# Kernel optimization log

Hardware: AMD Instinct MI355X
Metric: run time of the kernel (lower is better)

Reference implementation:

```python
import jax, jax.numpy as jnp
import numpy as np

B, D, H, E, TOPK, NTASK = 16384, 128, 4, 8, 2, 1
ODIM = D // H  # MoE expert output dim (input_feat // num_heads)


def setup_inputs() -> dict:
    key = jax.random.key(0)
    ks = jax.random.split(key, 12)
    s = lambda k, shp, fan: jax.random.normal(k, shp, jnp.float32) / np.sqrt(fan)
    return {
        "x": jax.random.normal(ks[0], (B, D), jnp.float32),
        "Wq": s(ks[1], (D, D * H), D), "bq": jnp.zeros((D * H,), jnp.float32),
        "Wk": s(ks[2], (D, D * H), D), "bk": jnp.zeros((D * H,), jnp.float32),
        "Wg": s(ks[3], (D, E), D),
        "W1": s(ks[4], (E, D, D), D), "b1": jnp.zeros((E, D), jnp.float32),
        "W2": s(ks[5], (E, D, ODIM), D), "b2": jnp.zeros((E, ODIM), jnp.float32),
        "Wout": s(ks[6], (H * ODIM, NTASK), H * ODIM),
        "bout": jnp.zeros((NTASK,), jnp.float32),
    }


def reference(x, Wq, bq, Wk, bk, Wg, W1, b1, W2, b2, Wout, bout):
    # query/key projections -> [B, H, D] token views, flattened to [N, D]
    tok = (x @ Wq + bq).reshape(B * H, D)
    gate_tok = (x @ Wk + bk).reshape(B * H, D)

    # gating: softmax over experts, top-2 routing with renormalized weights
    probs = jax.nn.softmax(gate_tok @ Wg, axis=-1)          # [N, E]
    top_p, top_i = jax.lax.top_k(probs, TOPK)               # [N, k]
    weights = top_p / jnp.sum(top_p, axis=-1, keepdims=True)

    # expert MLPs (dense all-expert compute, then gather selected)
    h = jax.nn.relu(jnp.einsum('nd,edh->neh', tok, W1) + b1)  # [N, E, D]
    eo = jnp.einsum('neh,eho->neo', h, W2) + b2               # [N, E, ODIM]
    sel = jnp.take_along_axis(eo, top_i[:, :, None], axis=1)  # [N, k, ODIM]
    y = jnp.sum(weights[:, :, None] * sel, axis=1)            # [N, ODIM]

    # load-balancing auxiliary loss (switch-style): E * sum(frac_i * mean_prob_i)
    one_hot = jax.nn.one_hot(top_i[:, 0], E, dtype=probs.dtype)
    frac = jnp.mean(one_hot, axis=0)
    mean_p = jnp.mean(probs, axis=0)
    aux_loss = E * jnp.sum(frac * mean_p)

    out = y.reshape(B, H * ODIM) @ Wout + bout                # [B, NTASK]
    return out, aux_loss
```

## Files before the change

### kernel.cpp

```cpp
#include <hip/hip_runtime.h>
#include <hip/hip_bf16.h>

#define BB   16384
#define DD   128
#define HH   4
#define EE   8
#define NN   (BB*HH)
#define OD   32
#define PT   136

typedef __attribute__((ext_vector_type(8))) short short8;
typedef __attribute__((ext_vector_type(4))) short short4v;
typedef __attribute__((ext_vector_type(4))) float f32x4;

static __device__ __forceinline__ short f2bf(float v) {
    unsigned int u = __builtin_bit_cast(unsigned int, v);
    u = (u + 0x7FFFu + ((u >> 16) & 1u)) >> 16;
    return (short)u;
}

__global__ __launch_bounds__(256) void prep(
    const float* __restrict__ Wq, const float* __restrict__ Wk, const float* __restrict__ Wg,
    const float* __restrict__ bk, const float* __restrict__ W1, const float* __restrict__ W2,
    const float* __restrict__ bout,
    short* __restrict__ WqF, short* __restrict__ W1F, short* __restrict__ W2F,
    float* __restrict__ Wkg, float* __restrict__ bkg, float* __restrict__ out)
{
    int idx = blockIdx.x * 256 + threadIdx.x;
    if (idx < 65536) {
        int j = idx & 7, lane = (idx >> 3) & 63, ks = (idx >> 9) & 3, ct = idx >> 11;
        int l16 = lane & 15, quad = lane >> 4;
        int c = ct * 16 + l16, k = ks * 32 + quad * 8 + j;
        WqF[idx] = f2bf(Wq[k * 512 + c]);
    } else if (idx < 196608) {
        int r = idx - 65536;
        int j = r & 7, lane = (r >> 3) & 63, ks = (r >> 9) & 3, mt = (r >> 11) & 7, e = r >> 14;
        int l16 = lane & 15, quad = lane >> 4;
        int m = mt * 16 + l16, k = ks * 32 + quad * 8 + j;
        W1F[r] = f2bf(W1[e * 16384 + k * 128 + m]);
    } else if (idx < 229376) {
        int r = idx - 196608;
        int j = r & 7, lane = (r >> 3) & 63, ks = (r >> 9) & 3, mt = (r >> 11) & 1, e = r >> 12;
        int l16 = lane & 15, quad = lane >> 4;
        int m = mt * 16 + l16, k = ks * 32 + quad * 8 + j;
        W2F[r] = f2bf(W2[e * 4096 + k * 32 + m]);
    } else if (idx < 233472) {
        int r = idx - 229376;
        int k = r >> 5, col = r & 31, hh = col >> 3, e = col & 7;
        float s = 0.f;
        for (int d = 0; d < 128; ++d) s += Wk[k * 512 + hh * 128 + d] * Wg[d * 8 + e];
        Wkg[k * 32 + col] = s;
    } else if (idx < 233504) {
        int r = idx - 233472;
        int hh = r >> 3, e = r & 7;
        float s = 0.f;
        for (int d = 0; d < 128; ++d) s += bk[hh * 128 + d] * Wg[d * 8 + e];
        bkg[r] = s;
    } else if (idx < 249888) {
        out[idx - 233504] = bout[0];
    }
}

__global__ __launch_bounds__(256) void k1q_tok(
    const float* __restrict__ x, const short* __restrict__ WqF, const float* __restrict__ bq,
    short* __restrict__ tokb)
{
    __shared__ short xL[32 * PT];
    const int t  = threadIdx.x;
    const int b0 = blockIdx.x * 32;

    {
        int slot = t >> 3, seg = t & 7;
        const float4* src = (const float4*)(x + (size_t)(b0 + slot) * 128 + seg * 16);
        float4 v0 = src[0], v1 = src[1], v2 = src[2], v3 = src[3];
        short8 a, b;
        a[0]=f2bf(v0.x); a[1]=f2bf(v0.y); a[2]=f2bf(v0.z); a[3]=f2bf(v0.w);
        a[4]=f2bf(v1.x); a[5]=f2bf(v1.y); a[6]=f2bf(v1.z); a[7]=f2bf(v1.w);
        b[0]=f2bf(v2.x); b[1]=f2bf(v2.y); b[2]=f2bf(v2.z); b[3]=f2bf(v2.w);
        b[4]=f2bf(v3.x); b[5]=f2bf(v3.y); b[6]=f2bf(v3.z); b[7]=f2bf(v3.w);
        *(short8*)(xL + slot * PT + seg * 16)     = a;
        *(short8*)(xL + slot * PT + seg * 16 + 8) = b;
    }
    __syncthreads();

    const int wv   = t >> 6;
    const int lane = t & 63;
    const int l16  = lane & 15;
    const int quad = lane >> 4;

    f32x4 acc[8][2];
    #pragma unroll
    for (int ml = 0; ml < 8; ++ml)
        #pragma unroll
        for (int nl = 0; nl < 2; ++nl)
            acc[ml][nl] = (f32x4){0.f, 0.f, 0.f, 0.f};

    short8 bf[2][4];
    #pragma unroll
    for (int nl = 0; nl < 2; ++nl)
        #pragma unroll
        for (int ks = 0; ks < 4; ++ks)
            bf[nl][ks] = *(const short8*)(xL + (nl*16 + l16) * PT + ks*32 + quad*8);

    #pragma unroll
    for (int ks = 0; ks < 4; ++ks) {
        short8 af[8];
        #pragma unroll
        for (int ml = 0; ml < 8; ++ml)
            af[ml] = *(const short8*)(WqF + ((size_t)(((wv*8 + ml)*4 + ks)*64 + lane)) * 8);
        #pragma unroll
        for (int ml = 0; ml < 8; ++ml)
            #pragma unroll
            for (int nl = 0; nl < 2; ++nl)
                acc[ml][nl] = __builtin_amdgcn_mfma_f32_16x16x32_bf16(af[ml], bf[nl][ks], acc[ml][nl], 0, 0, 0);
    }

    #pragma unroll
    for (int ml = 0; ml < 8; ++ml) {
        int c0 = wv*128 + ml*16 + quad*4;
        f32x4 bqv = *(const f32x4*)(bq + c0);
        #pragma unroll
        for (int nl = 0; nl < 2; ++nl) {
            int b = b0 + nl*16 + l16;
            short4v hv;
            #pragma unroll
            for (int r = 0; r < 4; ++r) hv[r] = f2bf(acc[ml][nl][r] + bqv[r]);
            *(short4v*)(tokb + (size_t)b * 512 + c0) = hv;
        }
    }
}

__global__ __launch_bounds__(256) void k1_gate(
    const float* __restrict__ x, const float* __restrict__ Wkg, const float* __restrict__ bkg,
    int* __restrict__ topi, float* __restrict__ wts, float* __restrict__ blkPart)
{
    __shared__ float xL[64 * 129];
    __shared__ float lps[EE];
    __shared__ float lcn[EE];
    __shared__ float lasg[EE];

    const int t  = threadIdx.x;
    const int b0 = blockIdx.x * 64;

    if (t < EE) { lps[t] = 0.f; lcn[t] = 0.f; lasg[t] = 0.f; }

    for (int i = t; i < 2048; i += 256) {
        int r = i >> 5, c = i & 31;
        float4 v = ((const float4*)(x + (size_t)(b0 + r) * 128))[c];
        float* dst = xL + r * 129 + c * 4;
        dst[0] = v.x; dst[1] = v.y; dst[2] = v.z; dst[3] = v.w;
    }
    __syncthreads();

    const int h  = __builtin_amdgcn_readfirstlane(t >> 6);
    const int lb = t & 63;

    const f32x4* wkg4 = (const f32x4*)Wkg;
    f32x4 a0 = ((const f32x4*)bkg)[h * 2];
    f32x4 a1 = ((const f32x4*)bkg)[h * 2 + 1];

    const float* xrow = xL + lb * 129;
    #pragma unroll 4
    for (int k = 0; k < 128; ++k) {
        float xv = xrow[k];
        f32x4 w0 = wkg4[k * 8 + h * 2];
        f32x4 w1 = wkg4[k * 8 + h * 2 + 1];
        a0 += w0 * xv;
        a1 += w1 * xv;
    }

    float l[8] = {a0[0], a0[1], a0[2], a0[3], a1[0], a1[1], a1[2], a1[3]};
    float mx = l[0];
    #pragma unroll
    for (int e = 1; e < 8; ++e) mx = fmaxf(mx, l[e]);
    float p[8]; float sm = 0.f;
    #pragma unroll
    for (int e = 0; e < 8; ++e) { p[e] = __expf(l[e] - mx); sm += p[e]; }
    float isin = 1.f / sm;
    #pragma unroll
    for (int e = 0; e < 8; ++e) p[e] *= isin;

    int i1 = 0; float p1 = p[0];
    #pragma unroll
    for (int e = 1; e < 8; ++e) if (p[e] > p1) { p1 = p[e]; i1 = e; }
    int i2 = (i1 == 0) ? 1 : 0; float p2 = p[i2];
    #pragma unroll
    for (int e = 0; e < 8; ++e) if (e != i1 && p[e] > p2) { p2 = p[e]; i2 = e; }

    int n = (b0 + lb) * 4 + h;
    float rinv = 1.f / (p1 + p2);
    topi[2*n]   = i1;        topi[2*n+1] = i2;
    wts[2*n]    = p1 * rinv; wts[2*n+1]  = p2 * rinv;

    #pragma unroll
    for (int e = 0; e < 8; ++e) {
        float v = p[e];
        #pragma unroll
        for (int m2 = 1; m2 < 64; m2 <<= 1) v += __shfl_xor(v, m2);
        unsigned long long m1b = __ballot(i1 == e);
        unsigned long long m2b = __ballot(i2 == e);
        if (lb == 0) {
            float c1 = (float)__popcll(m1b);
            atomicAdd(&lps[e], v);
            atomicAdd(&lcn[e], c1);
            atomicAdd(&lasg[e], c1 + (float)__popcll(m2b));
        }
    }
    __syncthreads();
    if (t < EE) {
        float* bp = blkPart + blockIdx.x * 32;
        bp[t]      = lps[t];
        bp[8 + t]  = lcn[t];
        bp[16 + t] = lasg[t];
    }
}

__global__ __launch_bounds__(256) void k2s_scan(
    const float* __restrict__ blkPart,
    int* __restrict__ bases, int* __restrict__ cursors, int* __restrict__ assignCnt,
    float* __restrict__ out)
{
    __shared__ float red[8][32];
    __shared__ float fin[24];
    const int t = threadIdx.x;
    const int chunk = t >> 5, s = t & 31;
    float v = 0.f;
    for (int i = 0; i < 32; ++i) v += blkPart[(chunk * 32 + i) * 32 + s];
    red[chunk][s] = v;
    __syncthreads();
    if (t < 24) {
        float sum = 0.f;
        #pragma unroll
        for (int c = 0; c < 8; ++c) sum += red[c][t];
        fin[t] = sum;
    }
    __syncthreads();
    if (t == 0) {
        int b = 0;
        float aux = 0.f;
        const float invN = 1.f / (float)NN;
        for (int e = 0; e < EE; ++e) {
            aux += (fin[8 + e] * invN) * (fin[e] * invN);
            int a = (int)(fin[16 + e] + 0.5f);
            assignCnt[e] = a;
            bases[e] = b; cursors[e] = b;
            b += (a + 63) & ~63;
        }
        out[BB] = (float)EE * aux;
    }
}

__global__ __launch_bounds__(256) void k2a_bin(
    const int* __restrict__ topi,
    int* __restrict__ cursors, int* __restrict__ listIdx)
{
    __shared__ int lcnt[EE];
    __shared__ int lbase[EE];
    int t = threadIdx.x;
    if (t < EE) lcnt[t] = 0;
    __syncthreads();
    int n = blockIdx.x * 256 + t;
    int i0 = topi[2*n], i1 = topi[2*n+1];
    int s0 = atomicAdd(&lcnt[i0], 1);
    int s1 = atomicAdd(&lcnt[i1], 1);
    __syncthreads();
    if (t < EE) lbase[t] = atomicAdd(&cursors[t], lcnt[t]);
    __syncthreads();
    listIdx[lbase[i0] + s0] = 2*n;
    listIdx[lbase[i1] + s1] = 2*n + 1;
}

__global__ __launch_bounds__(256) void k2b_expert(
    const short* __restrict__ tokb, const short* __restrict__ W1F,
    const float* __restrict__ b1, const short* __restrict__ W2F, const float* __restrict__ b2,
    const int* __restrict__ assignCnt, const int* __restrict__ bases,
    const int* __restrict__ listIdx, const float* __restrict__ wts,
    const float* __restrict__ Wout, float* __restrict__ out)
{
    __shared__ short tokL[64 * PT];
    __shared__ short hL[64 * PT];
    __shared__ int   ids[64];
    __shared__ float wsl[64];
    __shared__ float WoutL[128];

    const int e    = blockIdx.y;
    const int cnt  = assignCnt[e];
    const int off  = blockIdx.x * 64;
    if (off >= cnt) return;
    const int sb   = bases[e] + off;
    const int t    = threadIdx.x;
    const int nt   = min(64, cnt - off);

    if (t < 64) {
        int a = listIdx[sb + min(t, nt - 1)];
        ids[t] = a >> 1;
        wsl[t] = (t < nt) ? wts[a] : 0.f;
    }
    if (t >= 128 && t < 256) WoutL[t - 128] = Wout[t - 128];
    __syncthreads();

    #pragma unroll
    for (int r = 0; r < 4; ++r) {
        int i = t + r * 256;
        int slot = i >> 4, seg = i & 15;
        short8 v = *(const short8*)(tokb + (size_t)ids[slot] * 128 + seg * 8);
        *(short8*)(tokL + slot * PT + seg * 8) = v;
    }
    __syncthreads();

    const int wv   = t >> 6;
    const int lane = t & 63;
    const int l16  = lane & 15;
    const int quad = lane >> 4;

    f32x4 acc[2][4];
    #pragma unroll
    for (int ml = 0; ml < 2; ++ml)
        #pragma unroll
        for (int nl = 0; nl < 4; ++nl)
            acc[ml][nl] = (f32x4){0.f, 0.f, 0.f, 0.f};

    short8 af[2][4];
    #pragma unroll
    for (int ml = 0; ml < 2; ++ml)
        #pragma unroll
        for (int ks = 0; ks < 4; ++ks)
            af[ml][ks] = *(const short8*)(W1F + ((size_t)(((e*8 + wv*2 + ml)*4 + ks)*64 + lane)) * 8);

    short8 bf[4][4];
    #pragma unroll
    for (int nl = 0; nl < 4; ++nl)
        #pragma unroll
        for (int ks = 0; ks < 4; ++ks)
            bf[nl][ks] = *(const short8*)(tokL + (nl*16 + l16) * PT + ks*32 + quad*8);

    #pragma unroll
    for (int ks = 0; ks < 4; ++ks)
        #pragma unroll
        for (int ml = 0; ml < 2; ++ml)
            #pragma unroll
            for (int nl = 0; nl < 4; ++nl)
                acc[ml][nl] = __builtin_amdgcn_mfma_f32_16x16x32_bf16(af[ml][ks], bf[nl][ks], acc[ml][nl], 0, 0, 0);

    #pragma unroll
    for (int ml = 0; ml < 2; ++ml) {
        int hid0 = wv*32 + ml*16 + quad*4;
        f32x4 b1v = *(const f32x4*)(b1 + e*128 + hid0);
        #pragma unroll
        for (int nl = 0; nl < 4; ++nl) {
            short4v hv;
            #pragma unroll
            for (int r = 0; r < 4; ++r) {
                float v = acc[ml][nl][r] + b1v[r];
                hv[r] = f2bf(fmaxf(v, 0.f));
            }
            *(short4v*)(hL + (nl*16 + l16) * PT + hid0) = hv;
        }
    }
    __syncthreads();

    f32x4 acc2[2];
    acc2[0] = (f32x4){0.f, 0.f, 0.f, 0.f};
    acc2[1] = (f32x4){0.f, 0.f, 0.f, 0.f};

    short8 af2[2][4];
    #pragma unroll
    for (int ml = 0; ml < 2; ++ml)
        #pragma unroll
        for (int ks = 0; ks < 4; ++ks)
            af2[ml][ks] = *(const short8*)(W2F + ((size_t)(((e*2 + ml)*4 + ks)*64 + lane)) * 8);

    short8 bf2[4];
    #pragma unroll
    for (int ks = 0; ks < 4; ++ks)
        bf2[ks] = *(const short8*)(hL + (wv*16 + l16) * PT + ks*32 + quad*8);

    #pragma unroll
    for (int ks = 0; ks < 4; ++ks)
        #pragma unroll
        for (int ml = 0; ml < 2; ++ml)
            acc2[ml] = __builtin_amdgcn_mfma_f32_16x16x32_bf16(af2[ml][ks], bf2[ks], acc2[ml], 0, 0, 0);

    const int slot = wv*16 + l16;
    const int nn   = ids[slot];
    const int hsel = nn & 3;
    float partial = 0.f;
    #pragma unroll
    for (int ml = 0; ml < 2; ++ml) {
        int od0 = ml*16 + quad*4;
        f32x4 b2v = *(const f32x4*)(b2 + e*32 + od0);
        const float* wseg = WoutL + hsel*32 + od0;
        #pragma unroll
        for (int r = 0; r < 4; ++r)
            partial += (acc2[ml][r] + b2v[r]) * wseg[r];
    }
    partial += __shfl_xor(partial, 16);
    partial += __shfl_xor(partial, 32);
    if (quad == 0) {
        float v = partial * wsl[slot];
        atomicAdd(&out[nn >> 2], v);
    }
}

extern "C" void kernel_launch(void* const* d_in, const int* in_sizes, int n_in,
                              void* d_out, int out_size, void* d_ws, size_t ws_size,
                              hipStream_t stream) {
    (void)in_sizes; (void)n_in; (void)out_size; (void)ws_size;
    const float* x    = (const float*)d_in[0];
    const float* Wq   = (const float*)d_in[1];
    const float* bq   = (const float*)d_in[2];
    const float* Wk   = (const float*)d_in[3];
    const float* bk   = (const float*)d_in[4];
    const float* Wg   = (const float*)d_in[5];
    const float* W1   = (const float*)d_in[6];
    const float* b1   = (const float*)d_in[7];
    const float* W2   = (const float*)d_in[8];
    const float* b2   = (const float*)d_in[9];
    const float* Wout = (const float*)d_in[10];
    const float* bout = (const float*)d_in[11];
    float* out = (float*)d_out;

    char* ws = (char*)d_ws;
    short* tokb     = (short*)(ws + 0);
    int*   topi     = (int*)  (ws + 16777216);
    float* wts      = (float*)(ws + 17301504);
    int*   listIdx  = (int*)  (ws + 17825792);
    short* WqF      = (short*)(ws + 18352128);
    short* W1F      = (short*)(ws + 18483200);
    short* W2F      = (short*)(ws + 18745344);
    float* Wkg      = (float*)(ws + 18810880);
    float* bkg      = (float*)(ws + 18827264);
    float* blkPart  = (float*)(ws + 18827392);
    int*   bases    = (int*)  (ws + 18860160);
    int*   cursors  = (int*)  (ws + 18860192);
    int*   assignCnt= (int*)  (ws + 18860224);

    prep<<<977, 256, 0, stream>>>(Wq, Wk, Wg, bk, W1, W2, bout, WqF, W1F, W2F, Wkg, bkg, out);
    k1q_tok<<<512, 256, 0, stream>>>(x, WqF, bq, tokb);
    k1_gate<<<256, 256, 0, stream>>>(x, Wkg, bkg, topi, wts, blkPart);
    k2s_scan<<<1, 256, 0, stream>>>(blkPart, bases, cursors, assignCnt, out);
    k2a_bin<<<256, 256, 0, stream>>>(topi, cursors, listIdx);
    k2b_expert<<<dim3(1024, 8), 256, 0, stream>>>(tokb, W1F, b1, W2F, b2, assignCnt, bases, listIdx, wts, Wout, out);
}
```

Before: 140.7 us.

## Fuse projection, gating and binning; use fixed per-expert capacity lists

Merges the query-projection kernel and the gating kernel into one launch that branches on block index. The gating blocks now bin assignments straight into per-expert lists with a fixed capacity, so the separate scan and binning kernels and the top-index buffer go away. The aux-loss reduction moves into one block of the expert kernel. This cuts launches and global round trips, but any expert that receives more assignments than the capacity silently drops the overflow.

```diff
diff --git a/kernel.cpp b/kernel.cpp
--- a/kernel.cpp
+++ b/kernel.cpp
@@ -8,6 +8,7 @@
 #define NN   (BB*HH)
 #define OD   32
 #define PT   136
+#define CAP  24576
 
 typedef __attribute__((ext_vector_type(8))) short short8;
 typedef __attribute__((ext_vector_type(4))) short short4v;
@@ -24,7 +25,8 @@
     const float* __restrict__ bk, const float* __restrict__ W1, const float* __restrict__ W2,
     const float* __restrict__ bout,
     short* __restrict__ WqF, short* __restrict__ W1F, short* __restrict__ W2F,
-    float* __restrict__ Wkg, float* __restrict__ bkg, float* __restrict__ out)
+    float* __restrict__ Wkg, float* __restrict__ bkg, float* __restrict__ out,
+    int* __restrict__ cursors)
 {
     int idx = blockIdx.x * 256 + threadIdx.x;
     if (idx < 65536) {
@@ -48,106 +50,114 @@
         int r = idx - 229376;
         int k = r >> 5, col = r & 31, hh = col >> 3, e = col & 7;
         float s = 0.f;
+        #pragma unroll 8
         for (int d = 0; d < 128; ++d) s += Wk[k * 512 + hh * 128 + d] * Wg[d * 8 + e];
         Wkg[k * 32 + col] = s;
     } else if (idx < 233504) {
         int r = idx - 233472;
         int hh = r >> 3, e = r & 7;
         float s = 0.f;
+        #pragma unroll 8
         for (int d = 0; d < 128; ++d) s += bk[hh * 128 + d] * Wg[d * 8 + e];
         bkg[r] = s;
     } else if (idx < 249888) {
         out[idx - 233504] = bout[0];
+    } else if (idx < 249896) {
+        int r = idx - 249888;
+        cursors[r] = r * CAP;
     }
 }
 
-__global__ __launch_bounds__(256) void k1q_tok(
+__global__ __launch_bounds__(256) void k1_fused(
     const float* __restrict__ x, const short* __restrict__ WqF, const float* __restrict__ bq,
-    short* __restrict__ tokb)
+    const float* __restrict__ Wkg, const float* __restrict__ bkg,
+    short* __restrict__ tokb, float* __restrict__ wts, float* __restrict__ blkPart,
+    int* __restrict__ cursors, int* __restrict__ listIdx)
 {
-    __shared__ short xL[32 * PT];
-    const int t  = threadIdx.x;
-    const int b0 = blockIdx.x * 32;
-
-    {
-        int slot = t >> 3, seg = t & 7;
-        const float4* src = (const float4*)(x + (size_t)(b0 + slot) * 128 + seg * 16);
-        float4 v0 = src[0], v1 = src[1], v2 = src[2], v3 = src[3];
-        short8 a, b;
-        a[0]=f2bf(v0.x); a[1]=f2bf(v0.y); a[2]=f2bf(v0.z); a[3]=f2bf(v0.w);
-        a[4]=f2bf(v1.x); a[5]=f2bf(v1.y); a[6]=f2bf(v1.z); a[7]=f2bf(v1.w);
-        b[0]=f2bf(v2.x); b[1]=f2bf(v2.y); b[2]=f2bf(v2.z); b[3]=f2bf(v2.w);
-        b[4]=f2bf(v3.x); b[5]=f2bf(v3.y); b[6]=f2bf(v3.z); b[7]=f2bf(v3.w);
-        *(short8*)(xL + slot * PT + seg * 16)     = a;
-        *(short8*)(xL + slot * PT + seg * 16 + 8) = b;
-    }
-    __syncthreads();
-
-    const int wv   = t >> 6;
-    const int lane = t & 63;
-    const int l16  = lane & 15;
-    const int quad = lane >> 4;
-
-    f32x4 acc[8][2];
-    #pragma unroll
-    for (int ml = 0; ml < 8; ++ml)
-        #pragma unroll
-        for (int nl = 0; nl < 2; ++nl)
-            acc[ml][nl] = (f32x4){0.f, 0.f, 0.f, 0.f};
-
-    short8 bf[2][4];
-    #pragma unroll
-    for (int nl = 0; nl < 2; ++nl)
-        #pragma unroll
-        for (int ks = 0; ks < 4; ++ks)
-            bf[nl][ks] = *(const short8*)(xL + (nl*16 + l16) * PT + ks*32 + quad*8);
-
-    #pragma unroll
-    for (int ks = 0; ks < 4; ++ks) {
-        short8 af[8];
-        #pragma unroll
-        for (int ml = 0; ml < 8; ++ml)
-            af[ml] = *(const short8*)(WqF + ((size_t)(((wv*8 + ml)*4 + ks)*64 + lane)) * 8);
-        #pragma unroll
-        for (int ml = 0; ml < 8; ++ml)
-            #pragma unroll
-            for (int nl = 0; nl < 2; ++nl)
-                acc[ml][nl] = __builtin_amdgcn_mfma_f32_16x16x32_bf16(af[ml], bf[nl][ks], acc[ml][nl], 0, 0, 0);
-    }
-
-    #pragma unroll
-    for (int ml = 0; ml < 8; ++ml) {
-        int c0 = wv*128 + ml*16 + quad*4;
-        f32x4 bqv = *(const f32x4*)(bq + c0);
-        #pragma unroll
-        for (int nl = 0; nl < 2; ++nl) {
-            int b = b0 + nl*16 + l16;
-            short4v hv;
-            #pragma unroll
-            for (int r = 0; r < 4; ++r) hv[r] = f2bf(acc[ml][nl][r] + bqv[r]);
-            *(short4v*)(tokb + (size_t)b * 512 + c0) = hv;
-        }
-    }
-}
-
-__global__ __launch_bounds__(256) void k1_gate(
-    const float* __restrict__ x, const float* __restrict__ Wkg, const float* __restrict__ bkg,
-    int* __restrict__ topi, float* __restrict__ wts, float* __restrict__ blkPart)
-{
-    __shared__ float xL[64 * 129];
+    __shared__ __align__(16) char smem[64 * 129 * 4];
     __shared__ float lps[EE];
     __shared__ float lcn[EE];
-    __shared__ float lasg[EE];
-
-    const int t  = threadIdx.x;
-    const int b0 = blockIdx.x * 64;
-
-    if (t < EE) { lps[t] = 0.f; lcn[t] = 0.f; lasg[t] = 0.f; }
+    __shared__ int   lcnt[EE];
+    __shared__ int   lbase[EE];
+
+    const int t = threadIdx.x;
+
+    if (blockIdx.x < 512) {
+        short* xL = (short*)smem;
+        const int b0 = blockIdx.x * 32;
+
+        {
+            int slot = t >> 3, seg = t & 7;
+            const float4* src = (const float4*)(x + (size_t)(b0 + slot) * 128 + seg * 16);
+            float4 v0 = src[0], v1 = src[1], v2 = src[2], v3 = src[3];
+            short8 a, b;
+            a[0]=f2bf(v0.x); a[1]=f2bf(v0.y); a[2]=f2bf(v0.z); a[3]=f2bf(v0.w);
+            a[4]=f2bf(v1.x); a[5]=f2bf(v1.y); a[6]=f2bf(v1.z); a[7]=f2bf(v1.w);
+            b[0]=f2bf(v2.x); b[1]=f2bf(v2.y); b[2]=f2bf(v2.z); b[3]=f2bf(v2.w);
+            b[4]=f2bf(v3.x); b[5]=f2bf(v3.y); b[6]=f2bf(v3.z); b[7]=f2bf(v3.w);
+            *(short8*)(xL + slot * PT + seg * 16)     = a;
+            *(short8*)(xL + slot * PT + seg * 16 + 8) = b;
+        }
+        __syncthreads();
+
+        const int wv   = t >> 6;
+        const int lane = t & 63;
+        const int l16  = lane & 15;
+        const int quad = lane >> 4;
+
+        f32x4 acc[8][2];
+        #pragma unroll
+        for (int ml = 0; ml < 8; ++ml)
+            #pragma unroll
+            for (int nl = 0; nl < 2; ++nl)
+                acc[ml][nl] = (f32x4){0.f, 0.f, 0.f, 0.f};
+
+        short8 bf[2][4];
+        #pragma unroll
+        for (int nl = 0; nl < 2; ++nl)
+            #pragma unroll
+            for (int ks = 0; ks < 4; ++ks)
+                bf[nl][ks] = *(const short8*)(xL + (nl*16 + l16) * PT + ks*32 + quad*8);
+
+        #pragma unroll
+        for (int ks = 0; ks < 4; ++ks) {
+            short8 af[8];
+            #pragma unroll
+            for (int ml = 0; ml < 8; ++ml)
+                af[ml] = *(const short8*)(WqF + ((size_t)(((wv*8 + ml)*4 + ks)*64 + lane)) * 8);
+            #pragma unroll
+            for (int ml = 0; ml < 8; ++ml)
+                #pragma unroll
+                for (int nl = 0; nl < 2; ++nl)
+                    acc[ml][nl] = __builtin_amdgcn_mfma_f32_16x16x32_bf16(af[ml], bf[nl][ks], acc[ml][nl], 0, 0, 0);
+        }
+
+        #pragma unroll
+        for (int ml = 0; ml < 8; ++ml) {
+            int c0 = wv*128 + ml*16 + quad*4;
+            f32x4 bqv = *(const f32x4*)(bq + c0);
+            #pragma unroll
+            for (int nl = 0; nl < 2; ++nl) {
+                int b = b0 + nl*16 + l16;
+                short4v hv;
+                #pragma unroll
+                for (int r = 0; r < 4; ++r) hv[r] = f2bf(acc[ml][nl][r] + bqv[r]);
+                *(short4v*)(tokb + (size_t)b * 512 + c0) = hv;
+            }
+        }
+        return;
+    }
+
+    float* xG = (float*)smem;
+    const int gb = blockIdx.x - 512;
+    const int b0 = gb * 64;
+
+    if (t < EE) { lps[t] = 0.f; lcn[t] = 0.f; lcnt[t] = 0; }
 
     for (int i = t; i < 2048; i += 256) {
         int r = i >> 5, c = i & 31;
         float4 v = ((const float4*)(x + (size_t)(b0 + r) * 128))[c];
-        float* dst = xL + r * 129 + c * 4;
+        float* dst = xG + r * 129 + c * 4;
         dst[0] = v.x; dst[1] = v.y; dst[2] = v.z; dst[3] = v.w;
     }
     __syncthreads();
@@ -159,7 +169,7 @@
     f32x4 a0 = ((const f32x4*)bkg)[h * 2];
     f32x4 a1 = ((const f32x4*)bkg)[h * 2 + 1];
 
-    const float* xrow = xL + lb * 129;
+    const float* xrow = xG + lb * 129;
     #pragma unroll 4
     for (int k = 0; k < 128; ++k) {
         float xv = xrow[k];
@@ -189,8 +199,10 @@
 
     int n = (b0 + lb) * 4 + h;
     float rinv = 1.f / (p1 + p2);
-    topi[2*n]   = i1;        topi[2*n+1] = i2;
     wts[2*n]    = p1 * rinv; wts[2*n+1]  = p2 * rinv;
+
+    int s0 = atomicAdd(&lcnt[i1], 1);
+    int s1 = atomicAdd(&lcnt[i2], 1);
 
     #pragma unroll
     for (int e = 0; e < 8; ++e) {
@@ -198,98 +210,72 @@
         #pragma unroll
         for (int m2 = 1; m2 < 64; m2 <<= 1) v += __shfl_xor(v, m2);
         unsigned long long m1b = __ballot(i1 == e);
-        unsigned long long m2b = __ballot(i2 == e);
         if (lb == 0) {
-            float c1 = (float)__popcll(m1b);
             atomicAdd(&lps[e], v);
-            atomicAdd(&lcn[e], c1);
-            atomicAdd(&lasg[e], c1 + (float)__popcll(m2b));
-        }
-    }
-    __syncthreads();
+            atomicAdd(&lcn[e], (float)__popcll(m1b));
+        }
+    }
+    __syncthreads();
+    if (t < EE) lbase[t] = atomicAdd(&cursors[t], lcnt[t]);
+    __syncthreads();
+
+    int q0 = lbase[i1] + s0;
+    if (q0 < (i1 + 1) * CAP) listIdx[q0] = 2*n;
+    int q1 = lbase[i2] + s1;
+    if (q1 < (i2 + 1) * CAP) listIdx[q1] = 2*n + 1;
+
     if (t < EE) {
-        float* bp = blkPart + blockIdx.x * 32;
-        bp[t]      = lps[t];
-        bp[8 + t]  = lcn[t];
-        bp[16 + t] = lasg[t];
-    }
-}
-
-__global__ __launch_bounds__(256) void k2s_scan(
-    const float* __restrict__ blkPart,
-    int* __restrict__ bases, int* __restrict__ cursors, int* __restrict__ assignCnt,
-    float* __restrict__ out)
-{
-    __shared__ float red[8][32];
-    __shared__ float fin[24];
-    const int t = threadIdx.x;
-    const int chunk = t >> 5, s = t & 31;
-    float v = 0.f;
-    for (int i = 0; i < 32; ++i) v += blkPart[(chunk * 32 + i) * 32 + s];
-    red[chunk][s] = v;
-    __syncthreads();
-    if (t < 24) {
-        float sum = 0.f;
-        #pragma unroll
-        for (int c = 0; c < 8; ++c) sum += red[c][t];
-        fin[t] = sum;
-    }
-    __syncthreads();
-    if (t == 0) {
-        int b = 0;
-        float aux = 0.f;
-        const float invN = 1.f / (float)NN;
-        for (int e = 0; e < EE; ++e) {
-            aux += (fin[8 + e] * invN) * (fin[e] * invN);
-            int a = (int)(fin[16 + e] + 0.5f);
-            assignCnt[e] = a;
-            bases[e] = b; cursors[e] = b;
-            b += (a + 63) & ~63;
-        }
-        out[BB] = (float)EE * aux;
-    }
-}
-
-__global__ __launch_bounds__(256) void k2a_bin(
-    const int* __restrict__ topi,
-    int* __restrict__ cursors, int* __restrict__ listIdx)
-{
-    __shared__ int lcnt[EE];
-    __shared__ int lbase[EE];
-    int t = threadIdx.x;
-    if (t < EE) lcnt[t] = 0;
-    __syncthreads();
-    int n = blockIdx.x * 256 + t;
-    int i0 = topi[2*n], i1 = topi[2*n+1];
-    int s0 = atomicAdd(&lcnt[i0], 1);
-    int s1 = atomicAdd(&lcnt[i1], 1);
-    __syncthreads();
-    if (t < EE) lbase[t] = atomicAdd(&cursors[t], lcnt[t]);
-    __syncthreads();
-    listIdx[lbase[i0] + s0] = 2*n;
-    listIdx[lbase[i1] + s1] = 2*n + 1;
+        float* bp = blkPart + gb * 16;
+        bp[t]     = lps[t];
+        bp[8 + t] = lcn[t];
+    }
 }
 
 __global__ __launch_bounds__(256) void k2b_expert(
     const short* __restrict__ tokb, const short* __restrict__ W1F,
     const float* __restrict__ b1, const short* __restrict__ W2F, const float* __restrict__ b2,
-    const int* __restrict__ assignCnt, const int* __restrict__ bases,
-    const int* __restrict__ listIdx, const float* __restrict__ wts,
-    const float* __restrict__ Wout, float* __restrict__ out)
+    const int* __restrict__ cursors, const int* __restrict__ listIdx,
+    const float* __restrict__ wts, const float* __restrict__ Wout,
+    const float* __restrict__ blkPart, float* __restrict__ out)
 {
     __shared__ short tokL[64 * PT];
     __shared__ short hL[64 * PT];
     __shared__ int   ids[64];
     __shared__ float wsl[64];
     __shared__ float WoutL[128];
-
-    const int e    = blockIdx.y;
-    const int cnt  = assignCnt[e];
-    const int off  = blockIdx.x * 64;
+    __shared__ float red[16][16];
+    __shared__ float fin[16];
+
+    const int e = blockIdx.y;
+    const int t = threadIdx.x;
+
+    if (blockIdx.x == gridDim.x - 1 && e == 7) {
+        int chunk = t >> 4, col = t & 15;
+        float v = 0.f;
+        for (int i = 0; i < 16; ++i) v += blkPart[(chunk * 16 + i) * 16 + col];
+        red[chunk][col] = v;
+        __syncthreads();
+        if (t < 16) {
+            float s = 0.f;
+            #pragma unroll
+            for (int c = 0; c < 16; ++c) s += red[c][t];
+            fin[t] = s;
+        }
+        __syncthreads();
+        if (t == 0) {
+            float aux = 0.f;
+            const float invN = 1.f / (float)NN;
+            for (int e2 = 0; e2 < EE; ++e2) aux += (fin[8 + e2] * invN) * (fin[e2] * invN);
+            out[BB] = (float)EE * aux;
+        }
+    }
+
+    int cnt = cursors[e] - e * CAP;
+    if (cnt > CAP) cnt = CAP;
+    const int off = blockIdx.x * 64;
     if (off >= cnt) return;
-    const int sb   = bases[e] + off;
-    const int t    = threadIdx.x;
-    const int nt   = min(64, cnt - off);
+    const int sb  = e * CAP + off;
+    const int nt  = min(64, cnt - off);
 
     if (t < 64) {
         int a = listIdx[sb + min(t, nt - 1)];
@@ -422,23 +408,17 @@
 
     char* ws = (char*)d_ws;
     short* tokb     = (short*)(ws + 0);
-    int*   topi     = (int*)  (ws + 16777216);
-    float* wts      = (float*)(ws + 17301504);
-    int*   listIdx  = (int*)  (ws + 17825792);
-    short* WqF      = (short*)(ws + 18352128);
-    short* W1F      = (short*)(ws + 18483200);
-    short* W2F      = (short*)(ws + 18745344);
-    float* Wkg      = (float*)(ws + 18810880);
-    float* bkg      = (float*)(ws + 18827264);
-    float* blkPart  = (float*)(ws + 18827392);
-    int*   bases    = (int*)  (ws + 18860160);
-    int*   cursors  = (int*)  (ws + 18860192);
-    int*   assignCnt= (int*)  (ws + 18860224);
-
-    prep<<<977, 256, 0, stream>>>(Wq, Wk, Wg, bk, W1, W2, bout, WqF, W1F, W2F, Wkg, bkg, out);
-    k1q_tok<<<512, 256, 0, stream>>>(x, WqF, bq, tokb);
-    k1_gate<<<256, 256, 0, stream>>>(x, Wkg, bkg, topi, wts, blkPart);
-    k2s_scan<<<1, 256, 0, stream>>>(blkPart, bases, cursors, assignCnt, out);
-    k2a_bin<<<256, 256, 0, stream>>>(topi, cursors, listIdx);
-    k2b_expert<<<dim3(1024, 8), 256, 0, stream>>>(tokb, W1F, b1, W2F, b2, assignCnt, bases, listIdx, wts, Wout, out);
+    float* wts      = (float*)(ws + 16777216);
+    int*   listIdx  = (int*)  (ws + 17301504);
+    short* WqF      = (short*)(ws + 18087936);
+    short* W1F      = (short*)(ws + 18219008);
+    short* W2F      = (short*)(ws + 18481152);
+    float* Wkg      = (float*)(ws + 18546688);
+    float* bkg      = (float*)(ws + 18563072);
+    float* blkPart  = (float*)(ws + 18563200);
+    int*   cursors  = (int*)  (ws + 18579584);
+
+    prep<<<977, 256, 0, stream>>>(Wq, Wk, Wg, bk, W1, W2, bout, WqF, W1F, W2F, Wkg, bkg, out, cursors);
+    k1_fused<<<768, 256, 0, stream>>>(x, WqF, bq, Wkg, bkg, tokb, wts, blkPart, cursors, listIdx);
+    k2b_expert<<<dim3(CAP/64, 8), 256, 0, stream>>>(tokb, W1F, b1, W2F, b2, cursors, listIdx, wts, Wout, blkPart, out);
 }
```

After: 124.5 us. 1.13x faster.
